# Kernel tuning notes

Measured on AMD Instinct MI355X. Metric: run time of the kernel, lower is better.

The kernel has to match this reference:

```python
import jax, jax.numpy as jnp
import numpy as np

# Acoustic FDTD constants (seistorch-style geometry)
NSHOTS, NT = 4, 512
NZ, NX = 256, 256
NRECS = 128
DT = 1e-3   # s
DH = 10.0   # m grid spacing


def setup_inputs() -> dict:
    key = jax.random.key(0)
    k1, k2, k3, k4, k5, k6 = jax.random.split(key, 6)
    x = jax.random.normal(k1, (NSHOTS, NT), dtype=jnp.float32)  # source wavelets
    # velocity model in [1500, 4000] m/s (CFL: dt*vmax/dh = 0.4 < stability limit)
    vp = 1500.0 + 2500.0 * jax.random.uniform(k2, (NZ, NX), dtype=jnp.float32)
    src_z = jax.random.randint(k3, (NSHOTS,), 0, NZ)
    src_x = jax.random.randint(k4, (NSHOTS,), 0, NX)
    rec_z = jax.random.randint(k5, (NSHOTS, NRECS), 0, NZ)
    rec_x = jax.random.randint(k6, (NSHOTS, NRECS), 0, NX)
    return {"x": x, "vp": vp, "src_z": src_z, "src_x": src_x,
            "rec_z": rec_z, "rec_x": rec_x}


def _laplacian(p):
    # 5-point stencil, zero Dirichlet boundary. p: (B, NZ, NX)
    pp = jnp.pad(p, ((0, 0), (1, 1), (1, 1)))
    return (pp[:, 2:, 1:-1] + pp[:, :-2, 1:-1]
            + pp[:, 1:-1, 2:] + pp[:, 1:-1, :-2]
            - 4.0 * p) / (DH * DH)


def reference(x, vp, src_z, src_x, rec_z, rec_x):
    shots = jnp.arange(NSHOTS)
    c2dt2 = (vp * DT) ** 2  # (NZ, NX), broadcast over shots

    def step(carry, wav_t):
        p_prev, p = carry
        # 2nd-order acoustic update (the PDE "cell")
        p_next = 2.0 * p - p_prev + c2dt2 * _laplacian(p)
        # source scatter-inject (super_source)
        p_next = p_next.at[shots, src_z, src_x].add(wav_t * DT * DT)
        # receiver gather (super_probes): (NSHOTS, NRECS)
        rec = p_next[shots[:, None], rec_z, rec_x]
        return (p, p_next), rec

    p0 = jnp.zeros((NSHOTS, NZ, NX), dtype=x.dtype)
    _, recs = jax.lax.scan(step, (p0, p0), x.T)  # recs: (NT, NSHOTS, NRECS)
    # (shots, time, receivers, n_receiver_types=1)
    return jnp.transpose(recs, (1, 0, 2))[..., None]
```

## Files before the change

kernel.cpp:

```cpp
#include <hip/hip_runtime.h>

#define NSHOTS 4
#define NT     512
#define NZ     256
#define NX     256
#define NRECS  128

static constexpr float DTf    = 0.001f;
static constexpr float INVDH2 = 1.0f / (10.0f * 10.0f);

#define KSTEPS 16
#define TILE   32
#define RPT    8
#define NPAIRS 4
#define NWAVES 8
#define BLOCK  512
#define NWG    (NSHOTS * 64)
#define NPHASE (NT / KSTEPS)
#define LSTRIDE 32

typedef float v2f __attribute__((ext_vector_type(2)));

__device__ __forceinline__ float nbr_left(float v) {
  return __int_as_float(__builtin_amdgcn_update_dpp(
      0, __float_as_int(v), 0x138 , 0xf, 0xf, true));
}
__device__ __forceinline__ float nbr_right(float v) {
  return __int_as_float(__builtin_amdgcn_update_dpp(
      0, __float_as_int(v), 0x130 , 0xf, 0xf, true));
}

__device__ __forceinline__ float gload(const float* p) {
  return __hip_atomic_load(p, __ATOMIC_RELAXED, __HIP_MEMORY_SCOPE_AGENT);
}
__device__ __forceinline__ void gstore(float* p, float v) {
  __hip_atomic_store(p, v, __ATOMIC_RELAXED, __HIP_MEMORY_SCOPE_AGENT);
}
__device__ __forceinline__ unsigned fload(const unsigned* p) {
  return __hip_atomic_load(p, __ATOMIC_RELAXED, __HIP_MEMORY_SCOPE_AGENT);
}
__device__ __forceinline__ void fstore(unsigned* p, unsigned v) {
  __hip_atomic_store(p, v, __ATOMIC_RELAXED, __HIP_MEMORY_SCOPE_AGENT);
}

__global__ __launch_bounds__(BLOCK, 4) void wave_pk(
    float* __restrict__ f0c, float* __restrict__ f0p,
    float* __restrict__ f1c, float* __restrict__ f1p,
    const float* __restrict__ vp, const float* __restrict__ xwav,
    const int* __restrict__ src_z, const int* __restrict__ src_x,
    const int* __restrict__ rec_z, const int* __restrict__ rec_x,
    float* __restrict__ out,
    unsigned* __restrict__ bar)
{
  const int bid  = blockIdx.x;
  const int s    = bid >> 6;
  const int tz   = (bid >> 3) & 7;
  const int tx   = bid & 7;
  const int tid  = threadIdx.x;
  const int w    = tid >> 6;
  const int lane = tid & 63;

  const int gz0 = tz * TILE - KSTEPS;
  const int gx0 = tx * TILE - KSTEPS;
  const int gx  = gx0 + lane;
  const int zb  = w * RPT;

  __shared__ float haloTop[2][NWAVES][64];
  __shared__ float haloBot[2][NWAVES][64];
  __shared__ float recTile[2][TILE][TILE + 1];
  __shared__ int   cntS;
  __shared__ int   lzA[NRECS], lxA[NRECS];
  __shared__ unsigned pkA[NRECS];

  if (tid == 0) cntS = 0;
  __syncthreads();
  if (tid < NRECS) {
    const int lz = rec_z[s * NRECS + tid] - tz * TILE;
    const int lx = rec_x[s * NRECS + tid] - tx * TILE;
    lzA[tid] = lz; lxA[tid] = lx;
    if ((unsigned)lz < (unsigned)TILE && (unsigned)lx < (unsigned)TILE) {
      const int k = atomicAdd(&cntS, 1);
      pkA[k] = (unsigned)tid | ((unsigned)lz << 8) | ((unsigned)lx << 16);
    }
  }
  __syncthreads();
  const int nRec = cntS;
  int myR = 0, myLz = 0, myLx = 0;
  if (tid < nRec) {
    const unsigned p = pkA[tid];
    myR = p & 255; myLz = (p >> 8) & 31; myLx = (p >> 16) & 31;
  }
  const bool wbRow = (w >= 2 && w < 6) && (lane >= KSTEPS && lane < KSTEPS + TILE);
  const int  ilz   = (w - 2) * RPT;
  const int  ilx   = lane - KSTEPS;
  unsigned recMask = 0;
  if (wbRow) {
    for (int r = 0; r < NRECS; ++r)
      if (lxA[r] == ilx && (unsigned)(lzA[r] - ilz) < (unsigned)RPT)
        recMask |= 1u << (lzA[r] - ilz);
  }

  int nb = -1;
  if (tid < 8) {
    const int k  = (tid < 4) ? tid : tid + 1;
    const int dz = k / 3 - 1, dx = k % 3 - 1;
    const int qz = tz + dz, qx = tx + dx;
    if ((unsigned)qz < 8u && (unsigned)qx < 8u)
      nb = (s << 6) | (qz << 3) | qx;
  }
  unsigned* wF = bar;
  unsigned* rF = bar + (size_t)NWG * LSTRIDE;

  auto pollGE = [&](unsigned* base, unsigned target) {
    if (nb >= 0) {
      while (fload(base + (size_t)nb * LSTRIDE) < target)
        __builtin_amdgcn_s_sleep(1);
    }
  };

  const int slz = src_z[s] - gz0;
  const int slx = src_x[s] - gx0;
  const bool srcMine = (slx == lane) && ((unsigned)(slz - zb) < (unsigned)RPT);
  const int  srcI = slz - zb;
  v2f srcM2[NPAIRS];
  #pragma unroll
  for (int p = 0; p < NPAIRS; ++p) {
    srcM2[p].x = (srcMine && srcI == 2 * p)     ? 1.0f : 0.0f;
    srcM2[p].y = (srcMine && srcI == 2 * p + 1) ? 1.0f : 0.0f;
  }

  const bool xok = (unsigned)gx < (unsigned)NX;
  int   offRow[RPT];
  bool  okRow[RPT];
  v2f a2[NPAIRS], b2[NPAIRS], c22[NPAIRS], d22[NPAIRS];
  #pragma unroll
  for (int p = 0; p < NPAIRS; ++p) {
    #pragma unroll
    for (int h = 0; h < 2; ++h) {
      const int i  = 2 * p + h;
      const int gz = gz0 + zb + i;
      const bool ok = xok && ((unsigned)gz < (unsigned)NZ);
      okRow[i]  = ok;
      offRow[i] = ok ? ((s * NZ + gz) * NX + gx) : 0;
      float v = ok ? vp[gz * NX + gx] : 0.0f;
      v *= DTf;
      const float c2 = v * v * INVDH2;
      if (h == 0) { c22[p].x = c2; d22[p].x = 2.0f - 4.0f * c2; }
      else        { c22[p].y = c2; d22[p].y = 2.0f - 4.0f * c2; }
    }
    a2[p] = (v2f)(0.0f); b2[p] = (v2f)(0.0f);
  }

  #pragma unroll 1
  for (int ph = 0; ph < NPHASE; ++ph) {
    const int t0 = ph * KSTEPS;

    if (ph > 0) {
      pollGE(wF, (unsigned)ph);
      __syncthreads();
      const float* rc = (ph & 1) ? f0c : f1c;
      const float* rp = (ph & 1) ? f0p : f1p;
      if (!wbRow) {
        #pragma unroll
        for (int p = 0; p < NPAIRS; ++p) {
          a2[p].x = okRow[2 * p]     ? gload(rc + offRow[2 * p])     : 0.0f;
          a2[p].y = okRow[2 * p + 1] ? gload(rc + offRow[2 * p + 1]) : 0.0f;
          b2[p].x = okRow[2 * p]     ? gload(rp + offRow[2 * p])     : 0.0f;
          b2[p].y = okRow[2 * p + 1] ? gload(rp + offRow[2 * p + 1]) : 0.0f;
        }
      }
      __builtin_amdgcn_s_waitcnt(0);
      __syncthreads();
      if (tid == 0) fstore(rF + (size_t)bid * LSTRIDE, (unsigned)ph);
    }

    float amp[KSTEPS];
    {
      const float4* xw4 = (const float4*)(xwav + s * NT + t0);
      #pragma unroll
      for (int q = 0; q < KSTEPS / 4; ++q) {
        const float4 v = xw4[q];
        amp[4 * q + 0] = (v.x * DTf) * DTf;
        amp[4 * q + 1] = (v.y * DTf) * DTf;
        amp[4 * q + 2] = (v.z * DTf) * DTf;
        amp[4 * q + 3] = (v.w * DTf) * DTf;
      }
    }

    float recv[KSTEPS];

    auto do_step = [&](v2f (&cur)[NPAIRS], v2f (&nxt)[NPAIRS], int tau) {
      const int pb = tau & 1;
      haloTop[pb][w][lane] = cur[0].x;
      haloBot[pb][w][lane] = cur[NPAIRS - 1].y;
      __syncthreads();
      if (tau > 0 && tid < nRec) recv[tau - 1] = recTile[1 - pb][myLz][myLx];
      const float up0 = (w > 0)          ? haloBot[pb][w - 1][lane] : 0.0f;
      const float dn7 = (w < NWAVES - 1) ? haloTop[pb][w + 1][lane] : 0.0f;
      const v2f av = { amp[tau], amp[tau] };
      #pragma unroll
      for (int p = 0; p < NPAIRS; ++p) {
        const float cx = cur[p].x, cy = cur[p].y;
        const float upx = (p == 0)          ? up0 : cur[p - 1].y;
        const float dny = (p == NPAIRS - 1) ? dn7 : cur[p + 1].x;
        v2f ud, lr;
        ud.x = upx + cy;
        ud.y = cx + dny;
        lr.x = nbr_left(cx) + nbr_right(cx);
        lr.y = nbr_left(cy) + nbr_right(cy);
        const v2f sum = ud + lr;
        v2f t = __builtin_elementwise_fma(c22[p], sum, -nxt[p]);
        t = __builtin_elementwise_fma(d22[p], cur[p], t);
        t = __builtin_elementwise_fma(srcM2[p], av, t);
        nxt[p] = t;
      }
      if (recMask) {
        #pragma unroll
        for (int i = 0; i < RPT; ++i)
          if (recMask & (1u << i))
            recTile[pb][ilz + i][ilx] = (i & 1) ? nxt[i >> 1].y : nxt[i >> 1].x;
      }
    };

    #pragma unroll
    for (int h = 0; h < KSTEPS / 2; ++h) {
      do_step(a2, b2, 2 * h);
      do_step(b2, a2, 2 * h + 1);
    }

    if (ph >= 2 && ph != NPHASE - 1) pollGE(rF, (unsigned)(ph - 1));
    __syncthreads();
    if (tid < nRec) recv[KSTEPS - 1] = recTile[1][myLz][myLx];

    if (tid < nRec) {
      #pragma unroll
      for (int t = 0; t < KSTEPS; ++t)
        out[(s * NT + (t0 + t)) * NRECS + myR] = recv[t];
    }

    if (ph != NPHASE - 1) {
      float* wc = (ph & 1) ? f1c : f0c;
      float* wp = (ph & 1) ? f1p : f0p;
      if (wbRow) {
        #pragma unroll
        for (int p = 0; p < NPAIRS; ++p) {
          gstore(wc + offRow[2 * p],     a2[p].x);
          gstore(wc + offRow[2 * p + 1], a2[p].y);
          gstore(wp + offRow[2 * p],     b2[p].x);
          gstore(wp + offRow[2 * p + 1], b2[p].y);
        }
      }
      __builtin_amdgcn_s_waitcnt(0);
      __syncthreads();
      if (tid == 0) fstore(wF + (size_t)bid * LSTRIDE, (unsigned)(ph + 1));
    }
  }
}

extern "C" void kernel_launch(void* const* d_in, const int* in_sizes, int n_in,
                              void* d_out, int out_size, void* d_ws, size_t ws_size,
                              hipStream_t stream) {
  const float* x     = (const float*)d_in[0];
  const float* vp    = (const float*)d_in[1];
  const int*   src_z = (const int*)d_in[2];
  const int*   src_x = (const int*)d_in[3];
  const int*   rec_z = (const int*)d_in[4];
  const int*   rec_x = (const int*)d_in[5];
  float* out = (float*)d_out;

  float* ws = (float*)d_ws;
  const size_t F = (size_t)NSHOTS * NZ * NX;
  float* f0c = ws;
  float* f0p = ws + F;
  float* f1c = ws + 2 * F;
  float* f1p = ws + 3 * F;
  unsigned* bar = (unsigned*)(ws + 4 * F);

  hipMemsetAsync(bar, 0, 2 * (size_t)NWG * LSTRIDE * sizeof(unsigned), stream);

  wave_pk<<<dim3(NWG), dim3(BLOCK), 0, stream>>>(
      f0c, f0p, f1c, f1p, vp, x, src_z, src_x, rec_z, rec_x, out, bar);
}
```

Before: 323.4 us.

## Interleave two shots per workgroup to hide neighbor halo exchange latency

Each workgroup now owns tiles from two shots, shot s and s+2, with smaller 16x32 tiles and 6 rows per wave. It alternates the 16-step temporal blocks between them, so the global halo writeback, flag polling and reload for one shot overlap with compute on the other. The aim is to hide inter-workgroup synchronization stalls and global memory round trips behind useful work. In exchange, each tile carries a larger fraction of redundant halo computation (16-row core inside a 48-row region), register pressure goes up, and the flag protocol gets more complex, with more deadlock and ordering risk.

```diff
diff --git a/kernel.cpp b/kernel.cpp
--- a/kernel.cpp
+++ b/kernel.cpp
@@ -10,14 +10,19 @@
 static constexpr float INVDH2 = 1.0f / (10.0f * 10.0f);
 
 #define KSTEPS 16
-#define TILE   32
-#define RPT    8
-#define NPAIRS 4
+#define TILEX  32
+#define TILEZ  16
+#define RPT    6
+#define NPAIRS 3
 #define NWAVES 8
 #define BLOCK  512
-#define NWG    (NSHOTS * 64)
+#define NTZ    16
+#define NTX    8
+#define NTILES (NSHOTS * NTZ * NTX)
+#define NWG    256
 #define NPHASE (NT / KSTEPS)
 #define LSTRIDE 32
+#define SHOT2OFF (2 * NZ * NX)
 
 typedef float v2f __attribute__((ext_vector_type(2)));
 
@@ -43,7 +48,7 @@
   __hip_atomic_store(p, v, __ATOMIC_RELAXED, __HIP_MEMORY_SCOPE_AGENT);
 }
 
-__global__ __launch_bounds__(BLOCK, 4) void wave_pk(
+__global__ __launch_bounds__(BLOCK, 2) void wave_pk(
     float* __restrict__ f0c, float* __restrict__ f0p,
     float* __restrict__ f1c, float* __restrict__ f1p,
     const float* __restrict__ vp, const float* __restrict__ xwav,
@@ -53,86 +58,116 @@
     unsigned* __restrict__ bar)
 {
   const int bid  = blockIdx.x;
-  const int s    = bid >> 6;
-  const int tz   = (bid >> 3) & 7;
+  const int sA   = bid >> 7;
+  const int sB   = sA + 2;
+  const int tz   = (bid >> 3) & 15;
   const int tx   = bid & 7;
   const int tid  = threadIdx.x;
   const int w    = tid >> 6;
   const int lane = tid & 63;
 
-  const int gz0 = tz * TILE - KSTEPS;
-  const int gx0 = tx * TILE - KSTEPS;
+  const int gz0 = tz * TILEZ - KSTEPS;
+  const int gx0 = tx * TILEX - KSTEPS;
   const int gx  = gx0 + lane;
   const int zb  = w * RPT;
+  const int ilx = lane - KSTEPS;
+  const bool xin = (unsigned)ilx < (unsigned)TILEX;
 
   __shared__ float haloTop[2][NWAVES][64];
   __shared__ float haloBot[2][NWAVES][64];
-  __shared__ float recTile[2][TILE][TILE + 1];
+  __shared__ float recTile[2][TILEZ][TILEX + 1];
   __shared__ int   cntS;
-  __shared__ int   lzA[NRECS], lxA[NRECS];
-  __shared__ unsigned pkA[NRECS];
-
-  if (tid == 0) cntS = 0;
-  __syncthreads();
-  if (tid < NRECS) {
-    const int lz = rec_z[s * NRECS + tid] - tz * TILE;
-    const int lx = rec_x[s * NRECS + tid] - tx * TILE;
-    lzA[tid] = lz; lxA[tid] = lx;
-    if ((unsigned)lz < (unsigned)TILE && (unsigned)lx < (unsigned)TILE) {
-      const int k = atomicAdd(&cntS, 1);
-      pkA[k] = (unsigned)tid | ((unsigned)lz << 8) | ((unsigned)lx << 16);
-    }
-  }
-  __syncthreads();
-  const int nRec = cntS;
-  int myR = 0, myLz = 0, myLx = 0;
-  if (tid < nRec) {
-    const unsigned p = pkA[tid];
-    myR = p & 255; myLz = (p >> 8) & 31; myLx = (p >> 16) & 31;
-  }
-  const bool wbRow = (w >= 2 && w < 6) && (lane >= KSTEPS && lane < KSTEPS + TILE);
-  const int  ilz   = (w - 2) * RPT;
-  const int  ilx   = lane - KSTEPS;
-  unsigned recMask = 0;
-  if (wbRow) {
-    for (int r = 0; r < NRECS; ++r)
-      if (lxA[r] == ilx && (unsigned)(lzA[r] - ilz) < (unsigned)RPT)
-        recMask |= 1u << (lzA[r] - ilz);
-  }
-
-  int nb = -1;
+  __shared__ int   lzS[NRECS], lxS[NRECS];
+  __shared__ unsigned pkS[NRECS];
+
+  unsigned wbMask = 0;
+  if (xin) {
+    #pragma unroll
+    for (int i = 0; i < RPT; ++i)
+      if ((unsigned)(zb + i - KSTEPS) < (unsigned)TILEZ) wbMask |= 1u << i;
+  }
+
+  int nRecA = 0, nRecB = 0;
+  int myRA = 0, myLzA = 0, myLxA = 0;
+  int myRB = 0, myLzB = 0, myLxB = 0;
+  unsigned recMaskA = 0, recMaskB = 0;
+  #pragma unroll
+  for (int tt = 0; tt < 2; ++tt) {
+    const int s = tt ? sB : sA;
+    if (tid == 0) cntS = 0;
+    __syncthreads();
+    if (tid < NRECS) {
+      const int lz = rec_z[s * NRECS + tid] - tz * TILEZ;
+      const int lx = rec_x[s * NRECS + tid] - tx * TILEX;
+      lzS[tid] = lz; lxS[tid] = lx;
+      if ((unsigned)lz < (unsigned)TILEZ && (unsigned)lx < (unsigned)TILEX) {
+        const int k = atomicAdd(&cntS, 1);
+        pkS[k] = (unsigned)tid | ((unsigned)lz << 8) | ((unsigned)lx << 16);
+      }
+    }
+    __syncthreads();
+    const int n = cntS;
+    int mR = 0, mLz = 0, mLx = 0;
+    if (tid < n) {
+      const unsigned p = pkS[tid];
+      mR = p & 255; mLz = (p >> 8) & 31; mLx = (p >> 16) & 31;
+    }
+    unsigned rm = 0;
+    if (xin) {
+      for (int r = 0; r < NRECS; ++r)
+        if (lxS[r] == ilx && (unsigned)lzS[r] < (unsigned)TILEZ) {
+          const int i = lzS[r] - (zb - KSTEPS);
+          if ((unsigned)i < (unsigned)RPT) rm |= 1u << i;
+        }
+    }
+    __syncthreads();
+    if (tt == 0) { nRecA = n; myRA = mR; myLzA = mLz; myLxA = mLx; recMaskA = rm; }
+    else         { nRecB = n; myRB = mR; myLzB = mLz; myLxB = mLx; recMaskB = rm; }
+  }
+
+  int nbA = -1;
   if (tid < 8) {
     const int k  = (tid < 4) ? tid : tid + 1;
     const int dz = k / 3 - 1, dx = k % 3 - 1;
     const int qz = tz + dz, qx = tx + dx;
-    if ((unsigned)qz < 8u && (unsigned)qx < 8u)
-      nb = (s << 6) | (qz << 3) | qx;
-  }
-  unsigned* wF = bar;
-  unsigned* rF = bar + (size_t)NWG * LSTRIDE;
-
-  auto pollGE = [&](unsigned* base, unsigned target) {
+    if ((unsigned)qz < (unsigned)NTZ && (unsigned)qx < (unsigned)NTX)
+      nbA = (sA << 7) | (qz << 3) | qx;
+  }
+  const int nbB  = (nbA >= 0) ? nbA + 256 : -1;
+  const int idxA = (sA << 7) | (tz << 3) | tx;
+  const int idxB = idxA + 256;
+  unsigned* wFlg = bar;
+  unsigned* rFlg = bar + (size_t)NTILES * LSTRIDE;
+
+  auto pollGE = [&](unsigned* base, int nb, unsigned target) {
     if (nb >= 0) {
-      while (fload(base + (size_t)nb * LSTRIDE) < target)
-        __builtin_amdgcn_s_sleep(1);
+      const unsigned* p = base + (size_t)nb * LSTRIDE;
+      while (fload(p) < target) __builtin_amdgcn_s_sleep(1);
     }
   };
 
-  const int slz = src_z[s] - gz0;
-  const int slx = src_x[s] - gx0;
-  const bool srcMine = (slx == lane) && ((unsigned)(slz - zb) < (unsigned)RPT);
-  const int  srcI = slz - zb;
-  v2f srcM2[NPAIRS];
+  v2f srcM2A[NPAIRS], srcM2B[NPAIRS];
   #pragma unroll
-  for (int p = 0; p < NPAIRS; ++p) {
-    srcM2[p].x = (srcMine && srcI == 2 * p)     ? 1.0f : 0.0f;
-    srcM2[p].y = (srcMine && srcI == 2 * p + 1) ? 1.0f : 0.0f;
+  for (int tt = 0; tt < 2; ++tt) {
+    const int s   = tt ? sB : sA;
+    const int slz = src_z[s] - gz0;
+    const int slx = src_x[s] - gx0;
+    const bool mine = (slx == lane) && ((unsigned)(slz - zb) < (unsigned)RPT);
+    const int si = slz - zb;
+    #pragma unroll
+    for (int p = 0; p < NPAIRS; ++p) {
+      v2f m;
+      m.x = (mine && si == 2 * p)     ? 1.0f : 0.0f;
+      m.y = (mine && si == 2 * p + 1) ? 1.0f : 0.0f;
+      if (tt == 0) srcM2A[p] = m; else srcM2B[p] = m;
+    }
   }
 
   const bool xok = (unsigned)gx < (unsigned)NX;
   int   offRow[RPT];
   bool  okRow[RPT];
-  v2f a2[NPAIRS], b2[NPAIRS], c22[NPAIRS], d22[NPAIRS];
+  v2f c22[NPAIRS], d22[NPAIRS];
+  v2f a2A[NPAIRS], b2A[NPAIRS], a2B[NPAIRS], b2B[NPAIRS];
   #pragma unroll
   for (int p = 0; p < NPAIRS; ++p) {
     #pragma unroll
@@ -141,118 +176,158 @@
       const int gz = gz0 + zb + i;
       const bool ok = xok && ((unsigned)gz < (unsigned)NZ);
       okRow[i]  = ok;
-      offRow[i] = ok ? ((s * NZ + gz) * NX + gx) : 0;
+      offRow[i] = ok ? ((sA * NZ + gz) * NX + gx) : 0;
       float v = ok ? vp[gz * NX + gx] : 0.0f;
       v *= DTf;
       const float c2 = v * v * INVDH2;
       if (h == 0) { c22[p].x = c2; d22[p].x = 2.0f - 4.0f * c2; }
       else        { c22[p].y = c2; d22[p].y = 2.0f - 4.0f * c2; }
     }
-    a2[p] = (v2f)(0.0f); b2[p] = (v2f)(0.0f);
-  }
+    a2A[p] = (v2f)(0.0f); b2A[p] = (v2f)(0.0f);
+    a2B[p] = (v2f)(0.0f); b2B[p] = (v2f)(0.0f);
+  }
+
+  float amp[KSTEPS], recv[KSTEPS];
+
+  auto load_amp = [&](int s, int t0) {
+    const float4* xw4 = (const float4*)(xwav + s * NT + t0);
+    #pragma unroll
+    for (int q = 0; q < KSTEPS / 4; ++q) {
+      const float4 v = xw4[q];
+      amp[4 * q + 0] = (v.x * DTf) * DTf;
+      amp[4 * q + 1] = (v.y * DTf) * DTf;
+      amp[4 * q + 2] = (v.z * DTf) * DTf;
+      amp[4 * q + 3] = (v.w * DTf) * DTf;
+    }
+  };
+
+  auto do_step = [&](v2f (&cur)[NPAIRS], v2f (&nxt)[NPAIRS],
+                     const v2f (&sm)[NPAIRS], int tau,
+                     unsigned rMask, int nR, int mLz, int mLx) {
+    const int pb = tau & 1;
+    haloTop[pb][w][lane] = cur[0].x;
+    haloBot[pb][w][lane] = cur[NPAIRS - 1].y;
+    __syncthreads();
+    if (tau > 0 && tid < nR) recv[tau - 1] = recTile[1 - pb][mLz][mLx];
+    const float up0 = (w > 0)          ? haloBot[pb][w - 1][lane] : 0.0f;
+    const float dn  = (w < NWAVES - 1) ? haloTop[pb][w + 1][lane] : 0.0f;
+    const v2f av = { amp[tau], amp[tau] };
+    #pragma unroll
+    for (int p = 0; p < NPAIRS; ++p) {
+      const float cx = cur[p].x, cy = cur[p].y;
+      const float upx = (p == 0)          ? up0 : cur[p - 1].y;
+      const float dny = (p == NPAIRS - 1) ? dn  : cur[p + 1].x;
+      v2f ud, lr;
+      ud.x = upx + cy;
+      ud.y = cx + dny;
+      lr.x = nbr_left(cx) + nbr_right(cx);
+      lr.y = nbr_left(cy) + nbr_right(cy);
+      const v2f sum = ud + lr;
+      v2f t = __builtin_elementwise_fma(c22[p], sum, -nxt[p]);
+      t = __builtin_elementwise_fma(d22[p], cur[p], t);
+      t = __builtin_elementwise_fma(sm[p], av, t);
+      nxt[p] = t;
+    }
+    if (rMask) {
+      #pragma unroll
+      for (int i = 0; i < RPT; ++i)
+        if (rMask & (1u << i))
+          recTile[pb][zb + i - KSTEPS][ilx] = (i & 1) ? nxt[i >> 1].y : nxt[i >> 1].x;
+    }
+  };
 
   #pragma unroll 1
   for (int ph = 0; ph < NPHASE; ++ph) {
     const int t0 = ph * KSTEPS;
 
-    if (ph > 0) {
-      pollGE(wF, (unsigned)ph);
-      __syncthreads();
+    load_amp(sA, t0);
+    #pragma unroll
+    for (int hh = 0; hh < KSTEPS / 2; ++hh) {
+      do_step(a2A, b2A, srcM2A, 2 * hh,     recMaskA, nRecA, myLzA, myLxA);
+      do_step(b2A, a2A, srcM2A, 2 * hh + 1, recMaskA, nRecA, myLzA, myLxA);
+    }
+
+    if (ph >= 2 && ph < NPHASE - 1) pollGE(rFlg, nbA, (unsigned)(ph - 1));
+    if (ph >= 1)                    pollGE(wFlg, nbB, (unsigned)ph);
+    __syncthreads();
+    if (tid < nRecA) {
+      recv[KSTEPS - 1] = recTile[1][myLzA][myLxA];
+      #pragma unroll
+      for (int t = 0; t < KSTEPS; ++t)
+        out[(sA * NT + (t0 + t)) * NRECS + myRA] = recv[t];
+    }
+    if (ph < NPHASE - 1 && wbMask) {
+      float* wc = (ph & 1) ? f1c : f0c;
+      float* wp = (ph & 1) ? f1p : f0p;
+      #pragma unroll
+      for (int i = 0; i < RPT; ++i)
+        if (wbMask & (1u << i)) {
+          gstore(wc + offRow[i], (i & 1) ? a2A[i >> 1].y : a2A[i >> 1].x);
+          gstore(wp + offRow[i], (i & 1) ? b2A[i >> 1].y : b2A[i >> 1].x);
+        }
+    }
+    if (ph >= 1) {
       const float* rc = (ph & 1) ? f0c : f1c;
       const float* rp = (ph & 1) ? f0p : f1p;
-      if (!wbRow) {
+      #pragma unroll
+      for (int i = 0; i < RPT; ++i)
+        if (!(wbMask & (1u << i))) {
+          const float cv = okRow[i] ? gload(rc + offRow[i] + SHOT2OFF) : 0.0f;
+          const float pv = okRow[i] ? gload(rp + offRow[i] + SHOT2OFF) : 0.0f;
+          if (i & 1) { a2B[i >> 1].y = cv; b2B[i >> 1].y = pv; }
+          else       { a2B[i >> 1].x = cv; b2B[i >> 1].x = pv; }
+        }
+    }
+    load_amp(sB, t0);
+    __builtin_amdgcn_s_waitcnt(0);
+    __syncthreads();
+    if (tid == 0) {
+      if (ph < NPHASE - 1) fstore(wFlg + (size_t)idxA * LSTRIDE, (unsigned)(ph + 1));
+      if (ph >= 1)         fstore(rFlg + (size_t)idxB * LSTRIDE, (unsigned)ph);
+    }
+
+    #pragma unroll
+    for (int hh = 0; hh < KSTEPS / 2; ++hh) {
+      do_step(a2B, b2B, srcM2B, 2 * hh,     recMaskB, nRecB, myLzB, myLxB);
+      do_step(b2B, a2B, srcM2B, 2 * hh + 1, recMaskB, nRecB, myLzB, myLxB);
+    }
+
+    if (ph >= 2 && ph < NPHASE - 1) pollGE(rFlg, nbB, (unsigned)(ph - 1));
+    if (ph < NPHASE - 1)            pollGE(wFlg, nbA, (unsigned)(ph + 1));
+    __syncthreads();
+    if (tid < nRecB) {
+      recv[KSTEPS - 1] = recTile[1][myLzB][myLxB];
+      #pragma unroll
+      for (int t = 0; t < KSTEPS; ++t)
+        out[(sB * NT + (t0 + t)) * NRECS + myRB] = recv[t];
+    }
+    if (ph < NPHASE - 1) {
+      float* wc = (ph & 1) ? f1c : f0c;
+      float* wp = (ph & 1) ? f1p : f0p;
+      if (wbMask) {
         #pragma unroll
-        for (int p = 0; p < NPAIRS; ++p) {
-          a2[p].x = okRow[2 * p]     ? gload(rc + offRow[2 * p])     : 0.0f;
-          a2[p].y = okRow[2 * p + 1] ? gload(rc + offRow[2 * p + 1]) : 0.0f;
-          b2[p].x = okRow[2 * p]     ? gload(rp + offRow[2 * p])     : 0.0f;
-          b2[p].y = okRow[2 * p + 1] ? gload(rp + offRow[2 * p + 1]) : 0.0f;
+        for (int i = 0; i < RPT; ++i)
+          if (wbMask & (1u << i)) {
+            gstore(wc + offRow[i] + SHOT2OFF, (i & 1) ? a2B[i >> 1].y : a2B[i >> 1].x);
+            gstore(wp + offRow[i] + SHOT2OFF, (i & 1) ? b2B[i >> 1].y : b2B[i >> 1].x);
+          }
+      }
+      const float* rc = (ph & 1) ? f1c : f0c;
+      const float* rp = (ph & 1) ? f1p : f0p;
+      #pragma unroll
+      for (int i = 0; i < RPT; ++i)
+        if (!(wbMask & (1u << i))) {
+          const float cv = okRow[i] ? gload(rc + offRow[i]) : 0.0f;
+          const float pv = okRow[i] ? gload(rp + offRow[i]) : 0.0f;
+          if (i & 1) { a2A[i >> 1].y = cv; b2A[i >> 1].y = pv; }
+          else       { a2A[i >> 1].x = cv; b2A[i >> 1].x = pv; }
         }
-      }
       __builtin_amdgcn_s_waitcnt(0);
       __syncthreads();
-      if (tid == 0) fstore(rF + (size_t)bid * LSTRIDE, (unsigned)ph);
-    }
-
-    float amp[KSTEPS];
-    {
-      const float4* xw4 = (const float4*)(xwav + s * NT + t0);
-      #pragma unroll
-      for (int q = 0; q < KSTEPS / 4; ++q) {
-        const float4 v = xw4[q];
-        amp[4 * q + 0] = (v.x * DTf) * DTf;
-        amp[4 * q + 1] = (v.y * DTf) * DTf;
-        amp[4 * q + 2] = (v.z * DTf) * DTf;
-        amp[4 * q + 3] = (v.w * DTf) * DTf;
+      if (tid == 0) {
+        fstore(wFlg + (size_t)idxB * LSTRIDE, (unsigned)(ph + 1));
+        fstore(rFlg + (size_t)idxA * LSTRIDE, (unsigned)(ph + 1));
       }
-    }
-
-    float recv[KSTEPS];
-
-    auto do_step = [&](v2f (&cur)[NPAIRS], v2f (&nxt)[NPAIRS], int tau) {
-      const int pb = tau & 1;
-      haloTop[pb][w][lane] = cur[0].x;
-      haloBot[pb][w][lane] = cur[NPAIRS - 1].y;
-      __syncthreads();
-      if (tau > 0 && tid < nRec) recv[tau - 1] = recTile[1 - pb][myLz][myLx];
-      const float up0 = (w > 0)          ? haloBot[pb][w - 1][lane] : 0.0f;
-      const float dn7 = (w < NWAVES - 1) ? haloTop[pb][w + 1][lane] : 0.0f;
-      const v2f av = { amp[tau], amp[tau] };
-      #pragma unroll
-      for (int p = 0; p < NPAIRS; ++p) {
-        const float cx = cur[p].x, cy = cur[p].y;
-        const float upx = (p == 0)          ? up0 : cur[p - 1].y;
-        const float dny = (p == NPAIRS - 1) ? dn7 : cur[p + 1].x;
-        v2f ud, lr;
-        ud.x = upx + cy;
-        ud.y = cx + dny;
-        lr.x = nbr_left(cx) + nbr_right(cx);
-        lr.y = nbr_left(cy) + nbr_right(cy);
-        const v2f sum = ud + lr;
-        v2f t = __builtin_elementwise_fma(c22[p], sum, -nxt[p]);
-        t = __builtin_elementwise_fma(d22[p], cur[p], t);
-        t = __builtin_elementwise_fma(srcM2[p], av, t);
-        nxt[p] = t;
-      }
-      if (recMask) {
-        #pragma unroll
-        for (int i = 0; i < RPT; ++i)
-          if (recMask & (1u << i))
-            recTile[pb][ilz + i][ilx] = (i & 1) ? nxt[i >> 1].y : nxt[i >> 1].x;
-      }
-    };
-
-    #pragma unroll
-    for (int h = 0; h < KSTEPS / 2; ++h) {
-      do_step(a2, b2, 2 * h);
-      do_step(b2, a2, 2 * h + 1);
-    }
-
-    if (ph >= 2 && ph != NPHASE - 1) pollGE(rF, (unsigned)(ph - 1));
-    __syncthreads();
-    if (tid < nRec) recv[KSTEPS - 1] = recTile[1][myLz][myLx];
-
-    if (tid < nRec) {
-      #pragma unroll
-      for (int t = 0; t < KSTEPS; ++t)
-        out[(s * NT + (t0 + t)) * NRECS + myR] = recv[t];
-    }
-
-    if (ph != NPHASE - 1) {
-      float* wc = (ph & 1) ? f1c : f0c;
-      float* wp = (ph & 1) ? f1p : f0p;
-      if (wbRow) {
-        #pragma unroll
-        for (int p = 0; p < NPAIRS; ++p) {
-          gstore(wc + offRow[2 * p],     a2[p].x);
-          gstore(wc + offRow[2 * p + 1], a2[p].y);
-          gstore(wp + offRow[2 * p],     b2[p].x);
-          gstore(wp + offRow[2 * p + 1], b2[p].y);
-        }
-      }
-      __builtin_amdgcn_s_waitcnt(0);
-      __syncthreads();
-      if (tid == 0) fstore(wF + (size_t)bid * LSTRIDE, (unsigned)(ph + 1));
     }
   }
 }
@@ -276,7 +351,7 @@
   float* f1p = ws + 3 * F;
   unsigned* bar = (unsigned*)(ws + 4 * F);
 
-  hipMemsetAsync(bar, 0, 2 * (size_t)NWG * LSTRIDE * sizeof(unsigned), stream);
+  hipMemsetAsync(bar, 0, 2 * (size_t)NTILES * LSTRIDE * sizeof(unsigned), stream);
 
   wave_pk<<<dim3(NWG), dim3(BLOCK), 0, stream>>>(
       f0c, f0p, f1c, f1p, vp, x, src_z, src_x, rec_z, rec_x, out, bar);
```

Result: slower. 460.5 us (+42.4%).
